# Kernel optimization log

Hardware: AMD Instinct MI355X
Metric: run time of the kernel (lower is better)

## Reference

```python
import jax, jax.numpy as jnp
import numpy as np

# dims: batch, cdd_size, his_size, signal_length, embedding_dim, filter_num, top-k, levels, vocab
B, CDD, HIS, S, E, F, K, L, VOCAB = 32, 5, 50, 20, 300, 150, 30, 3, 50000


def _conv1d(x, w, b, d):
    # x: [N, C_in, S], w: [C_out, C_in, 3], 'same' length via padding=d, dilation=d
    y = jax.lax.conv_general_dilated(x, w, (1,), [(d, d)], rhs_dilation=(d,),
                                     dimension_numbers=('NCW', 'OIW', 'NCW'))
    return y + b[None, :, None]


def _conv3d(x, w, b):
    # x: [N, C_in, D, H, W], padding 1 on all spatial dims
    y = jax.lax.conv_general_dilated(x, w, (1, 1, 1), [(1, 1)] * 3,
                                     dimension_numbers=('NCDHW', 'OIDHW', 'NCDHW'))
    return y + b[None, :, None, None, None]


def _maxpool3(x):
    return jax.lax.reduce_window(x, -jnp.inf, jax.lax.max,
                                 (1, 1, 3, 3, 3), (1, 1, 3, 3, 3), 'VALID')


def setup_inputs() -> dict:
    key = jax.random.key(0)
    ks = jax.random.split(key, 12)
    n = lambda k, s, sc=0.05: jax.random.normal(k, s, dtype=jnp.float32) * sc
    return {
        'candidate_title': jax.random.randint(ks[0], (B, CDD, S), 0, VOCAB),
        'clicked_title': jax.random.randint(ks[1], (B, HIS, S), 0, VOCAB),
        'his_mask': jnp.zeros((B, HIS, 1), dtype=bool),
        'embedding': n(ks[2], (VOCAB, E), 0.1),
        'w1': n(ks[3], (F, E, 3)), 'b1': jnp.zeros((F,), jnp.float32),
        'w2': n(ks[4], (F, F, 3)), 'b2': jnp.zeros((F,), jnp.float32),
        'w3': n(ks[5], (F, F, 3)), 'b3': jnp.zeros((F,), jnp.float32),
        'ln_w': jnp.ones((F,), jnp.float32), 'ln_b': jnp.zeros((F,), jnp.float32),
        'q_words': n(ks[6], (1, F), 1.0), 'q_levels': n(ks[7], (1, F), 1.0),
        'c3d_w1': n(ks[8], (32, L, 3, 3, 3)), 'c3d_b1': jnp.zeros((32,), jnp.float32),
        'c3d_w2': n(ks[9], (16, 32, 3, 3, 3)), 'c3d_b2': jnp.zeros((16,), jnp.float32),
        'ltr_w': n(ks[10], (1, 192)), 'ltr_b': jnp.zeros((1,), jnp.float32),
    }


def reference(candidate_title, clicked_title, his_mask, embedding,
              w1, b1, w2, b2, w3, b3, ln_w, ln_b, q_words, q_levels,
              c3d_w1, c3d_b1, c3d_w2, c3d_b2, ltr_w, ltr_b):
    def ln(x):
        m = x.mean(-1, keepdims=True)
        v = x.var(-1, keepdims=True)  # biased var, matches torch LayerNorm
        return (x - m) / jnp.sqrt(v + 1e-5) * ln_w + ln_b

    scale_e = jnp.sqrt(jnp.float32(E))  # NOTE: original divides by sqrt(embedding_dim)

    def encode(ids):
        nn = ids.shape[1]
        x = embedding[ids].reshape(-1, S, E).transpose(0, 2, 1)  # [N, E, S] (dropout = identity at eval)
        d1 = ln(_conv1d(x, w1, b1, 1).transpose(0, 2, 1))                     # [N, S, F]
        d2 = ln(_conv1d(d1.transpose(0, 2, 1), w2, b2, 2).transpose(0, 2, 1))
        d3 = ln(_conv1d(d2.transpose(0, 2, 1), w3, b3, 3).transpose(0, 2, 1))
        dil = jnp.stack([jax.nn.relu(d1), jax.nn.relu(d2), jax.nn.relu(d3)], axis=2)  # [N, S, L, F]
        dil = dil.reshape(B, nn, S, L, F)
        # level attention with query_levels
        lw = jax.nn.softmax(jnp.einsum('bnslf,f->bnsl', dil, q_levels[0]) / scale_e, axis=-1)
        wf = jnp.einsum('bnsl,bnslf->bnsf', lw, dil)
        # word attention with query_words
        ww = jax.nn.softmax(jnp.einsum('bnsf,f->bns', wf, q_words[0]) / scale_e, axis=-1)
        reprs = jnp.einsum('bns,bnsf->bnf', ww, wf)
        return dil, reprs

    cdd_emb, cdd_repr = encode(candidate_title)   # [B,CDD,S,L,F], [B,CDD,F]
    his_emb, his_repr = encode(clicked_title)     # [B,HIS,S,L,F], [B,HIS,F]

    # news-level attention -> top-k one-hot gating (gather of history news)
    scores = jnp.einsum('bcf,bhf->bch', cdd_repr, his_repr)
    scores = jnp.where(his_mask.transpose(0, 2, 1), -jnp.inf, scores)
    attn = jax.nn.softmax(scores, axis=-1)
    _, idx = jax.lax.top_k(attn, K)                                  # [B,CDD,K]
    his_act = his_emb[jnp.arange(B)[:, None, None], idx]             # [B,CDD,K,S,L,F]

    # fusion tensor: per-level word-word interaction maps
    cdd_t = cdd_emb.transpose(0, 1, 3, 2, 4)       # [B,CDD,L,S,F]
    his_t = his_act.transpose(0, 1, 2, 4, 3, 5)    # [B,CDD,K,L,S,F]
    fusion = jnp.einsum('bclsf,bckltf->bcklst', cdd_t, his_t) / jnp.sqrt(jnp.float32(F))
    fusion = fusion.reshape(B * CDD, K, L, S, S).transpose(0, 2, 1, 3, 4)  # [B*CDD, L, K, S, S]

    h = _maxpool3(jax.nn.relu(_conv3d(fusion, c3d_w1, c3d_b1)))
    h = _maxpool3(jax.nn.relu(_conv3d(h, c3d_w2, c3d_b2)))
    feat = h.reshape(B, CDD, -1)                   # [B, CDD, 192]
    score = jnp.einsum('bcd,d->bc', feat, ltr_w[0]) + ltr_b[0]
    return jax.nn.log_softmax(score, axis=-1)
```

## Files before the change

### kernel.cpp

```cpp
#include <hip/hip_runtime.h>
#include <hip/hip_bf16.h>

#define NB   32
#define NCDD 5
#define NHIS 50
#define SS   20
#define EE   300
#define FF   150
#define KK   30
#define LL   3
#define NSEQ (NB*NCDD + NB*NHIS)
#define NCD  (NB*NCDD)
#define NROW (NSEQ*SS)
#define CONVGRID (NROW/64)

typedef unsigned short u16;
typedef __attribute__((ext_vector_type(8))) short bf16x8;
typedef __attribute__((ext_vector_type(4))) float f32x4;
typedef __attribute__((ext_vector_type(4))) unsigned int u32x4;

__device__ __forceinline__ float b2f(u16 v) {
    union { unsigned int u; float f; } c; c.u = ((unsigned int)v) << 16; return c.f;
}
__device__ __forceinline__ u16 f2b(float f) {
    union { float f; unsigned int u; } c; c.f = f;
    unsigned int r = c.u + 0x7FFF + ((c.u >> 16) & 1);
    return (u16)(r >> 16);
}
__device__ __forceinline__ float ldf(const void* p, size_t i, int isbf) {
    return isbf ? b2f(((const u16*)p)[i]) : ((const float*)p)[i];
}
__device__ __forceinline__ float dget(const float* d, size_t i) {
    unsigned int u = ((const unsigned int*)d)[i];
    return b2f((u16)(u & 0xffffu)) + b2f((u16)(u >> 16));
}
__device__ __forceinline__ bf16x8 ld_frag8(const u16* p) {
    uint2 q0 = *(const uint2*)(p);
    uint2 q1 = *(const uint2*)(p + 4);
    u32x4 t; t.x = q0.x; t.y = q0.y; t.z = q1.x; t.w = q1.y;
    return __builtin_bit_cast(bf16x8, t);
}

__global__ void detect_dtype(const u16* lnw_raw, int* flag) {
    if (threadIdx.x == 0)
        flag[0] = (lnw_raw[0] == 0x3F80 && lnw_raw[1] == 0x3F80) ? 1 : 0;
}

struct CJob { const void* src; float* dst; int n; };
struct CJobs { CJob j[13]; };

__global__ __launch_bounds__(256) void convert_many(CJobs jobs, const int* flagp) {
    int isbf = flagp[0];
    CJob job = jobs.j[blockIdx.x];
    for (int i = threadIdx.x; i < job.n; i += 256) job.dst[i] = ldf(job.src, i, isbf);
}

__global__ __launch_bounds__(256) void repack_wb(const void* w, const int* flagp,
                                                 u16* outh, u16* outl,
                                                 int CIN, int KP, int CV) {
    int isbf = flagp[0];
    int i = blockIdx.x*256 + threadIdx.x;
    if (i >= 160*3*KP) return;
    int g = i % KP; int r = i / KP; int tap = r % 3; int f = r / 3;
    float v = 0.f;
    if (f < FF && g < CV) v = ldf(w, ((size_t)f*CIN + g)*3 + tap, isbf);
    u16 hi = f2b(v);
    u16 lo = f2b(v - b2f(hi));
    size_t o = (size_t)f*(3*KP) + (size_t)tap*KP + g;
    outh[o] = hi; outl[o] = lo;
}

__global__ __launch_bounds__(256) void repack_w1c(const void* w, const int* flagp,
                                                  u16* outh, u16* outl) {
    int isbf = flagp[0];
    int i = blockIdx.x*256 + threadIdx.x;
    if (i >= 3*32*32) return;
    int k = i & 31; int oc = (i >> 5) & 31; int kx = i >> 10;
    float v = 0.f;
    if (k < 27) {
        int kz = k / 9, r = k - kz*9, ky = r / 3, ic = r - ky*3;
        v = ldf(w, ((((size_t)oc*3 + ic)*3 + kz)*3 + ky)*3 + kx, isbf);
    }
    u16 hi = f2b(v); u16 lo = f2b(v - b2f(hi));
    outh[i] = hi; outl[i] = lo;
}

__global__ __launch_bounds__(256) void repack_w2(const void* w, const int* flagp,
                                                 u16* outh, u16* outl) {
    int isbf = flagp[0];
    int i = blockIdx.x*256 + threadIdx.x;
    if (i >= 16*864) return;
    int ic = i & 31; int r = i >> 5; int tap = r % 27; int oc = r / 27;
    float v = ldf(w, ((size_t)oc*32 + ic)*27 + tap, isbf);
    u16 hi = f2b(v); u16 lo = f2b(v - b2f(hi));
    size_t o = (size_t)oc*864 + tap*32 + ic;
    outh[o] = hi; outl[o] = lo;
}

template<int STAGE>
__global__ __launch_bounds__(256) void conv_mfma(const int* __restrict__ flagp,
        const int* __restrict__ cand, const int* __restrict__ clik,
        const void* __restrict__ emb,
        const unsigned int* __restrict__ dprev,
        const u16* __restrict__ wh, const u16* __restrict__ wl,
        const float* __restrict__ bias,
        const float* __restrict__ lnw, const float* __restrict__ lnb,
        unsigned int* __restrict__ dout)
{
    constexpr int KC  = 32;
    constexpr int PAD = 40;
    constexpr int KT  = (STAGE == 0) ? 960 : 480;
    constexpr int NC  = KT / KC;
    constexpr int DIL = (STAGE == 1) ? 2 : 3;
    constexpr int ASZ = 64*PAD, BSZ = 160*PAD;
    constexpr int STG = (2*ASZ + 2*BSZ)*2;
    constexpr int SMB = (STG > 64*164*4) ? STG : 64*164*4;
    __shared__ __align__(16) char smem[SMB];
    u16* Ah = (u16*)smem;
    u16* Al = Ah + ASZ;
    u16* Bh = Al + ASZ;
    u16* Bl = Bh + BSZ;

    const int tid  = threadIdx.x;
    const int row0 = blockIdx.x * 64;
    const int lane = tid & 63, wid = tid >> 6;
    const int wm = wid >> 1, wn = wid & 1;
    const int lr = lane & 15, lk = lane >> 4;
    const int isbf = flagp[0];

    const int arow = tid >> 2, aseg = tid & 3;
    const int grow = row0 + arow;
    const int an   = grow / 20;
    const int as   = grow - an*20;
    int aid[3];
    if constexpr (STAGE == 0) {
        #pragma unroll
        for (int t = 0; t < 3; ++t) {
            int w = as + t - 1;
            aid[t] = ((unsigned)w < 20u) ? ((an < NCD) ? cand[an*SS + w] : clik[(an - NCD)*SS + w])
                                         : -1;
        }
    }

    float xa[8];
    uint4 ra32[2];
    uint4 rb[5];

    auto LOADG = [&](int c) {
        if constexpr (STAGE == 0) {
            int tap = c / 10;
            int e0  = (c - tap*10)*32 + aseg*8;
            int id  = aid[tap];
            float4 x0 = {0.f,0.f,0.f,0.f}, x1 = {0.f,0.f,0.f,0.f};
            if (id >= 0) {
                if (!isbf) {
                    const float* ep = (const float*)emb + (size_t)id*EE + e0;
                    if (e0 < EE)     x0 = *(const float4*)ep;
                    if (e0 + 4 < EE) x1 = *(const float4*)(ep + 4);
                } else {
                    const u16* ep = (const u16*)emb + (size_t)id*EE + e0;
                    float t[8];
                    #pragma unroll
                    for (int j = 0; j < 8; ++j) t[j] = (e0 + j < EE) ? b2f(ep[j]) : 0.f;
                    x0.x=t[0]; x0.y=t[1]; x0.z=t[2]; x0.w=t[3];
                    x1.x=t[4]; x1.y=t[5]; x1.z=t[6]; x1.w=t[7];
                }
            }
            xa[0]=x0.x; xa[1]=x0.y; xa[2]=x0.z; xa[3]=x0.w;
            xa[4]=x1.x; xa[5]=x1.y; xa[6]=x1.z; xa[7]=x1.w;
        } else {
            int tap = c / 5;
            int f0  = (c - tap*5)*32;
            int word = as + DIL*(tap - 1);
            int gbase = f0 + aseg*8;
            ra32[0].x=ra32[0].y=ra32[0].z=ra32[0].w=0u;
            ra32[1].x=ra32[1].y=ra32[1].z=ra32[1].w=0u;
            if ((unsigned)word < 20u && gbase < FF) {
                const unsigned int* p = dprev + (size_t)(an*SS + word)*FF + gbase;
                uint2 q0 = *(const uint2*)(p);
                uint2 q1 = *(const uint2*)(p + 2);
                uint2 q2 = *(const uint2*)(p + 4);
                uint2 q3 = *(const uint2*)(p + 6);
                ra32[0].x = q0.x; ra32[0].y = q0.y; ra32[0].z = q1.x; ra32[0].w = q1.y;
                ra32[1].x = q2.x; ra32[1].y = q2.y; ra32[1].z = q3.x; ra32[1].w = q3.y;
                if (gbase + 7 >= FF) {
                    if (gbase + 1 >= FF) ra32[0].y = 0u;
                    if (gbase + 2 >= FF) ra32[0].z = 0u;
                    if (gbase + 3 >= FF) ra32[0].w = 0u;
                    if (gbase + 4 >= FF) ra32[1].x = 0u;
                    if (gbase + 5 >= FF) ra32[1].y = 0u;
                    if (gbase + 6 >= FF) ra32[1].z = 0u;
                    ra32[1].w = 0u;
                }
            }
        }
        #pragma unroll
        for (int j = 0; j < 5; ++j) {
            int item = tid + j*256;
            const u16* wp = (item < 640) ? wh : wl;
            int rem  = (item < 640) ? item : item - 640;
            rb[j] = *(const uint4*)(wp + (size_t)(rem >> 2)*KT + c*KC + (rem & 3)*8);
        }
    };

    auto WRITE = [&]() {
        uint4 h, l;
        if constexpr (STAGE == 0) {
            u16 hh[8], lo[8];
            #pragma unroll
            for (int j = 0; j < 8; ++j) {
                hh[j] = f2b(xa[j]);
                lo[j] = f2b(xa[j] - b2f(hh[j]));
            }
            h.x = hh[0] | ((unsigned)hh[1] << 16); h.y = hh[2] | ((unsigned)hh[3] << 16);
            h.z = hh[4] | ((unsigned)hh[5] << 16); h.w = hh[6] | ((unsigned)hh[7] << 16);
            l.x = lo[0] | ((unsigned)lo[1] << 16); l.y = lo[2] | ((unsigned)lo[3] << 16);
            l.z = lo[4] | ((unsigned)lo[5] << 16); l.w = lo[6] | ((unsigned)lo[7] << 16);
        } else {
            h.x = (ra32[0].x & 0xffffu) | (ra32[0].y << 16);
            h.y = (ra32[0].z & 0xffffu) | (ra32[0].w << 16);
            h.z = (ra32[1].x & 0xffffu) | (ra32[1].y << 16);
            h.w = (ra32[1].z & 0xffffu) | (ra32[1].w << 16);
            l.x = (ra32[0].x >> 16) | (ra32[0].y & 0xffff0000u);
            l.y = (ra32[0].z >> 16) | (ra32[0].w & 0xffff0000u);
            l.z = (ra32[1].x >> 16) | (ra32[1].y & 0xffff0000u);
            l.w = (ra32[1].z >> 16) | (ra32[1].w & 0xffff0000u);
        }
        *(uint4*)(Ah + arow*PAD + aseg*8) = h;
        *(uint4*)(Al + arow*PAD + aseg*8) = l;
        #pragma unroll
        for (int j = 0; j < 5; ++j) {
            int item = tid + j*256;
            u16* bp = (item < 640) ? Bh : Bl;
            int rem = (item < 640) ? item : item - 640;
            *(uint4*)(bp + (rem >> 2)*PAD + (rem & 3)*8) = rb[j];
        }
    };

    f32x4 acc[2][5];
    #pragma unroll
    for (int mf = 0; mf < 2; ++mf)
        #pragma unroll
        for (int nf = 0; nf < 5; ++nf)
            acc[mf][nf] = (f32x4){0.f,0.f,0.f,0.f};

    auto COMPUTE = [&]() {
        bf16x8 fah[2], fal[2], fbh[5], fbl[5];
        #pragma unroll
        for (int mf = 0; mf < 2; ++mf) {
            fah[mf] = *(const bf16x8*)(Ah + (wm*32 + mf*16 + lr)*PAD + lk*8);
            fal[mf] = *(const bf16x8*)(Al + (wm*32 + mf*16 + lr)*PAD + lk*8);
        }
        #pragma unroll
        for (int nf = 0; nf < 5; ++nf) {
            fbh[nf] = *(const bf16x8*)(Bh + (wn*80 + nf*16 + lr)*PAD + lk*8);
            fbl[nf] = *(const bf16x8*)(Bl + (wn*80 + nf*16 + lr)*PAD + lk*8);
        }
        #pragma unroll
        for (int mf = 0; mf < 2; ++mf)
            #pragma unroll
            for (int nf = 0; nf < 5; ++nf)
                acc[mf][nf] = __builtin_amdgcn_mfma_f32_16x16x32_bf16(fah[mf], fbh[nf], acc[mf][nf], 0, 0, 0);
        #pragma unroll
        for (int mf = 0; mf < 2; ++mf)
            #pragma unroll
            for (int nf = 0; nf < 5; ++nf)
                acc[mf][nf] = __builtin_amdgcn_mfma_f32_16x16x32_bf16(fah[mf], fbl[nf], acc[mf][nf], 0, 0, 0);
        #pragma unroll
        for (int mf = 0; mf < 2; ++mf)
            #pragma unroll
            for (int nf = 0; nf < 5; ++nf)
                acc[mf][nf] = __builtin_amdgcn_mfma_f32_16x16x32_bf16(fal[mf], fbh[nf], acc[mf][nf], 0, 0, 0);
    };

    LOADG(0); WRITE();
    for (int c = 0; c < NC; ++c) {
        if (c + 1 < NC) LOADG(c + 1);
        __syncthreads();
        COMPUTE();
        __syncthreads();
        if (c + 1 < NC) WRITE();
    }

    float* outb = (float*)smem;
    #pragma unroll
    for (int mf = 0; mf < 2; ++mf)
        #pragma unroll
        for (int nf = 0; nf < 5; ++nf)
            #pragma unroll
            for (int r = 0; r < 4; ++r)
                outb[(wm*32 + mf*16 + lk*4 + r)*164 + wn*80 + nf*16 + lr] = acc[mf][nf][r];
    __syncthreads();

    for (int rl = wid*16; rl < wid*16 + 16; ++rl) {
        float vv[3]; float sum = 0.f, sq = 0.f;
        #pragma unroll
        for (int j = 0; j < 3; ++j) {
            int f = lane + j*64;
            float v = 0.f;
            if (f < FF) v = outb[rl*164 + f] + bias[f];
            vv[j] = v; sum += v; sq += v*v;
        }
        #pragma unroll
        for (int off = 32; off; off >>= 1) { sum += __shfl_down(sum, off); sq += __shfl_down(sq, off); }
        sum = __shfl(sum, 0); sq = __shfl(sq, 0);
        float m = sum / FF, var = sq / FF - m*m, inv = rsqrtf(var + 1e-5f);
        #pragma unroll
        for (int j = 0; j < 3; ++j) {
            int f = lane + j*64;
            if (f < FF) {
                float v = (vv[j] - m) * inv * lnw[f] + lnb[f];
                u16 hi = f2b(v);
                unsigned int lo = (unsigned int)f2b(v - b2f(hi));
                dout[(size_t)(row0 + rl)*FF + f] = (unsigned int)hi | (lo << 16);
            }
        }
    }
}

__global__ __launch_bounds__(256) void lvwd_attn(const float* d1, const float* d2, const float* d3,
                                                 const float* ql, const float* qw, float* reprs) {
    __shared__ float wfs[SS*FF];
    __shared__ float scs[SS];
    int n = blockIdx.x, tid = threadIdx.x;
    int wave = tid >> 6, lane = tid & 63;
    for (int s = wave; s < SS; s += 4) {
        size_t base = ((size_t)n*SS + s) * FF;
        float v[3][3];
        float dt[3] = {0.f, 0.f, 0.f};
        #pragma unroll
        for (int j = 0; j < 3; ++j) {
            int f = lane + j*64;
            float q = (f < FF) ? ql[f] : 0.f;
            float x0 = (f < FF) ? fmaxf(dget(d1, base+f), 0.f) : 0.f;
            float x1 = (f < FF) ? fmaxf(dget(d2, base+f), 0.f) : 0.f;
            float x2 = (f < FF) ? fmaxf(dget(d3, base+f), 0.f) : 0.f;
            v[0][j] = x0; v[1][j] = x1; v[2][j] = x2;
            dt[0] += x0*q; dt[1] += x1*q; dt[2] += x2*q;
        }
        #pragma unroll
        for (int off = 32; off; off >>= 1) {
            dt[0] += __shfl_xor(dt[0], off);
            dt[1] += __shfl_xor(dt[1], off);
            dt[2] += __shfl_xor(dt[2], off);
        }
        const float sc = 0.057735026918962584f;
        float a0 = dt[0]*sc, a1 = dt[1]*sc, a2 = dt[2]*sc;
        float mx = fmaxf(a0, fmaxf(a1, a2));
        float e0 = expf(a0-mx), e1 = expf(a1-mx), e2 = expf(a2-mx);
        float den = e0+e1+e2;
        float l0 = e0/den, l1 = e1/den, l2 = e2/den;
        #pragma unroll
        for (int j = 0; j < 3; ++j) {
            int f = lane + j*64;
            if (f < FF) wfs[s*FF + f] = l0*v[0][j] + l1*v[1][j] + l2*v[2][j];
        }
    }
    __syncthreads();
    if (wave == 0) {
        if (lane < SS) {
            float a = 0.f;
            for (int f = 0; f < FF; ++f) a += wfs[lane*FF + f]*qw[f];
            scs[lane] = a * 0.057735026918962584f;
        }
        float mx = -1e30f;
        #pragma unroll
        for (int s = 0; s < SS; ++s) mx = fmaxf(mx, scs[s]);
        float ww[SS]; float den = 0.f;
        #pragma unroll
        for (int s = 0; s < SS; ++s) { ww[s] = expf(scs[s]-mx); den += ww[s]; }
        float inv = 1.f/den;
        for (int f = lane; f < FF; f += 64) {
            float a = 0.f;
            #pragma unroll
            for (int s = 0; s < SS; ++s) a += ww[s]*wfs[s*FF + f];
            reprs[(size_t)n*FF + f] = a*inv;
        }
    }
}

__global__ __launch_bounds__(256) void score_kernel(const float* reprs, const unsigned char* mask,
                                                    float* scores) {
    int i = blockIdx.x*256 + threadIdx.x;
    if (i >= NB*NCDD*NHIS) return;
    int b = i/(NCDD*NHIS); int r = i%(NCDD*NHIS); int h = r%NHIS; int c = r/NHIS;
    const float* cr = reprs + (size_t)(b*NCDD + c)*FF;
    const float* hr = reprs + (size_t)(NCD + b*NHIS + h)*FF;
    float a = 0.f;
    for (int f = 0; f < FF; ++f) a += cr[f]*hr[f];
    if (mask[b*NHIS + h]) a = -1e30f;
    scores[i] = a;
}

__global__ __launch_bounds__(64) void topk_kernel(const float* scores, int* idx) {
    int i = blockIdx.x*64 + threadIdx.x;
    if (i >= NB*NCDD) return;
    float sc[NHIS];
    const float* sp = scores + i*NHIS;
    for (int h = 0; h < NHIS; ++h) sc[h] = sp[h];
    for (int k = 0; k < KK; ++k) {
        int best = 0; float bv = -1e38f;
        for (int h = 0; h < NHIS; ++h) { if (sc[h] > bv) { bv = sc[h]; best = h; } }
        idx[i*KK + k] = best;
        sc[best] = -1e38f;
    }
}

__global__ __launch_bounds__(256) void fusion_kernel(const float* d1, const float* d2, const float* d3,
                                                     const int* idx, unsigned int* fusp) {
    constexpr int RS  = 168;
    constexpr int TSZ = 32*RS;
    __shared__ __align__(16) u16 smem[4*TSZ];
    u16* Ah = smem;
    u16* Al = smem + TSZ;
    u16* Hh = smem + 2*TSZ;
    u16* Hl = smem + 3*TSZ;
    int blk = blockIdx.x;
    int k = blk % KK; int r2 = blk / KK; int l = r2 % LL; int bc = r2 / LL;
    int b = bc / NCDD;
    int nh = NCD + b*NHIS + idx[bc*KK + k];
    const float* dl = (l == 0) ? d1 : ((l == 1) ? d2 : d3);
    const unsigned int* Ap = (const unsigned int*)dl + (size_t)bc*SS*FF;
    const unsigned int* Hp = (const unsigned int*)dl + (size_t)nh*SS*FF;
    int tid = threadIdx.x;
    for (int i = tid; i < 4*TSZ/8; i += 256)
        *(uint4*)(smem + (size_t)i*8) = (uint4){0u,0u,0u,0u};
    __syncthreads();
    for (int item = tid; item < 760; item += 256) {
        int side = item >= 380;
        int rem  = side ? item - 380 : item;
        int row  = rem / 19, f0 = (rem - row*19)*8;
        const unsigned int* p = (side ? Hp : Ap) + row*FF + f0;
        unsigned int q[8];
        #pragma unroll
        for (int j = 0; j < 8; j += 2) {
            uint2 t2 = {0u, 0u};
            if (f0 + j < FF) t2 = *(const uint2*)(p + j);
            q[j] = t2.x; q[j+1] = t2.y;
        }
        unsigned int hh[8], ll[8];
        #pragma unroll
        for (int j = 0; j < 8; ++j) {
            unsigned int u = q[j];
            float f = b2f((u16)(u & 0xffffu)) + b2f((u16)(u >> 16));
            int keep = (f > 0.f);
            hh[j] = keep ? (u & 0xffffu) : 0u;
            ll[j] = keep ? (u >> 16)     : 0u;
        }
        uint4 h, lo;
        h.x  = hh[0] | (hh[1] << 16); h.y  = hh[2] | (hh[3] << 16);
        h.z  = hh[4] | (hh[5] << 16); h.w  = hh[6] | (hh[7] << 16);
        lo.x = ll[0] | (ll[1] << 16); lo.y = ll[2] | (ll[3] << 16);
        lo.z = ll[4] | (ll[5] << 16); lo.w = ll[6] | (ll[7] << 16);
        u16* dh = (side ? Hh : Ah) + row*RS + f0;
        u16* dL = (side ? Hl : Al) + row*RS + f0;
        *(uint4*)dh = h;
        *(uint4*)dL = lo;
    }
    __syncthreads();
    const int lane = tid & 63, wid = tid >> 6;
    const int wm = wid >> 1, wn = wid & 1;
    const int lr = lane & 15, lk = lane >> 4;
    f32x4 acc = {0.f, 0.f, 0.f, 0.f};
    #pragma unroll
    for (int c = 0; c < 5; ++c) {
        bf16x8 fah = *(const bf16x8*)(Ah + (wm*16 + lr)*RS + c*32 + lk*8);
        bf16x8 fal = *(const bf16x8*)(Al + (wm*16 + lr)*RS + c*32 + lk*8);
        bf16x8 fbh = *(const bf16x8*)(Hh + (wn*16 + lr)*RS + c*32 + lk*8);
        bf16x8 fbl = *(const bf16x8*)(Hl + (wn*16 + lr)*RS + c*32 + lk*8);
        acc = __builtin_amdgcn_mfma_f32_16x16x32_bf16(fah, fbh, acc, 0, 0, 0);
        acc = __builtin_amdgcn_mfma_f32_16x16x32_bf16(fah, fbl, acc, 0, 0, 0);
        acc = __builtin_amdgcn_mfma_f32_16x16x32_bf16(fal, fbh, acc, 0, 0, 0);
    }
    #pragma unroll
    for (int r = 0; r < 4; ++r) {
        int s = wm*16 + lk*4 + r, t = wn*16 + lr;
        if (s < SS && t < SS) {
            float v = acc[r] * 0.08164965809277261f;
            u16 hi = f2b(v);
            unsigned int lo = (unsigned int)f2b(v - b2f(hi));
            fusp[(size_t)blk*400 + s*20 + t] = (unsigned int)hi | (lo << 16);
        }
    }
}

#define C1RS 36
__global__ __launch_bounds__(256) void c3d1_mfma(const unsigned int* __restrict__ fusp,
                                                 const u16* __restrict__ wh,
                                                 const u16* __restrict__ wl,
                                                 const float* __restrict__ bias,
                                                 unsigned int* __restrict__ h1p) {
    __shared__ __align__(16) u16 Ah[209*C1RS];
    __shared__ __align__(16) u16 Al[209*C1RS];
    __shared__ int mb[18*32];
    int blk = blockIdx.x;
    int yh = blk & 1; int r0 = blk >> 1; int g = r0 % 10; int bc = r0 / 10;
    int tid = threadIdx.x;
    for (int i = tid; i < 18*32; i += 256) mb[i] = 0;
    for (int i = tid; i < 209*C1RS; i += 256) { Ah[i] = 0; Al[i] = 0; }
    const int lane = tid & 63, wid = tid >> 6;
    const int lr = lane & 15, lk = lane >> 4;
    const float b0 = bias[lr], b1 = bias[16 + lr];
    const int p  = tid;
    const int yp = p / 22, cx = p - yp*22;
    const int gx = cx - 1;
    const int yb = yh*9 + yp - 1;
    const bool prow = (p < 198);
    const bool gxok = ((unsigned)gx < 20u);

    for (int zi = 0; zi < 3; ++zi) {
        int z = g*3 + zi;
        __syncthreads();
        if (p < 208) {
            #pragma unroll
            for (int k = 0; k < 27; ++k) {
                const int kz = k / 9, r2 = k - kz*9, ky = r2 / 3, ic = r2 - ky*3;
                int zz = z + kz - 1;
                int gy = yb + ky;
                unsigned int u = 0;
                if (prow && gxok && (unsigned)gy < 20u && (unsigned)zz < 30u)
                    u = fusp[((size_t)(bc*3 + ic)*30 + zz)*400 + gy*20 + gx];
                Ah[p*C1RS + k] = (u16)(u & 0xffffu);
                Al[p*C1RS + k] = (u16)(u >> 16);
            }
        }
        __syncthreads();
        f32x4 acc[4][2];
        #pragma unroll
        for (int fi = 0; fi < 4; ++fi) { acc[fi][0] = (f32x4){0,0,0,0}; acc[fi][1] = (f32x4){0,0,0,0}; }
        #pragma unroll
        for (int kx = 0; kx < 3; ++kx) {
            bf16x8 bh0 = *(const bf16x8*)(wh + kx*1024 + lr*32 + lk*8);
            bf16x8 bl0 = *(const bf16x8*)(wl + kx*1024 + lr*32 + lk*8);
            bf16x8 bh1 = *(const bf16x8*)(wh + kx*1024 + (16 + lr)*32 + lk*8);
            bf16x8 bl1 = *(const bf16x8*)(wl + kx*1024 + (16 + lr)*32 + lk*8);
            #pragma unroll
            for (int fi = 0; fi < 4; ++fi) {
                int frag = wid + fi*4;
                if (frag >= 13) break;
                int pp = frag*16 + lr + (kx - 1);
                int adr = (pp < 0 ? 0 : pp)*C1RS + lk*8;
                bf16x8 ah = ld_frag8(Ah + adr);
                bf16x8 al = ld_frag8(Al + adr);
                acc[fi][0] = __builtin_amdgcn_mfma_f32_16x16x32_bf16(ah, bh0, acc[fi][0], 0, 0, 0);
                acc[fi][0] = __builtin_amdgcn_mfma_f32_16x16x32_bf16(ah, bl0, acc[fi][0], 0, 0, 0);
                acc[fi][0] = __builtin_amdgcn_mfma_f32_16x16x32_bf16(al, bh0, acc[fi][0], 0, 0, 0);
                acc[fi][1] = __builtin_amdgcn_mfma_f32_16x16x32_bf16(ah, bh1, acc[fi][1], 0, 0, 0);
                acc[fi][1] = __builtin_amdgcn_mfma_f32_16x16x32_bf16(ah, bl1, acc[fi][1], 0, 0, 0);
                acc[fi][1] = __builtin_amdgcn_mfma_f32_16x16x32_bf16(al, bh1, acc[fi][1], 0, 0, 0);
            }
        }
        #pragma unroll
        for (int fi = 0; fi < 4; ++fi) {
            int frag = wid + fi*4;
            if (frag >= 13) break;
            #pragma unroll
            for (int r4 = 0; r4 < 4; ++r4) {
                int pc = frag*16 + lk*4 + r4;
                if (pc >= 198) continue;
                int ypc = pc / 22, cxc = pc - ypc*22;
                int gxc = cxc - 1;
                if ((unsigned)gxc < 18u) {
                    int cell = (ypc/3)*6 + gxc/3;
                    float v0 = fmaxf(acc[fi][0][r4] + b0, 0.f);
                    float v1 = fmaxf(acc[fi][1][r4] + b1, 0.f);
                    atomicMax(&mb[cell*32 + lr],      __float_as_int(v0));
                    atomicMax(&mb[cell*32 + 16 + lr], __float_as_int(v1));
                }
            }
        }
    }
    __syncthreads();
    for (int i = tid; i < 18*32; i += 256) {
        int oc = i & 31, cell = i >> 5;
        int dyl = cell / 6, dx = cell - dyl*6;
        int dydx = (yh*3 + dyl)*6 + dx;
        float v = __int_as_float(mb[i]);
        u16 hi = f2b(v);
        unsigned int lo = (unsigned int)f2b(v - b2f(hi));
        h1p[((size_t)(bc*10 + g)*36 + dydx)*32 + oc] = (unsigned int)hi | (lo << 16);
    }
}

#define ARS 36
#define APL (36*ARS)
__global__ __launch_bounds__(256) void c3d2_kernel(const unsigned int* __restrict__ h1p,
                                                   const u16* __restrict__ wh,
                                                   const u16* __restrict__ wl,
                                                   const float* __restrict__ bias,
                                                   float* __restrict__ h2) {
    __shared__ __align__(16) u16 Ah[12*APL];
    __shared__ __align__(16) u16 Al[12*APL];
    int bc = blockIdx.x, tid = threadIdx.x;
    for (int i = tid; i < 2*APL; i += 256) {
        int a = (i < APL) ? i : (11*APL + i - APL);
        Ah[a] = 0; Al[a] = 0;
    }
    for (int i = tid; i < 10*36*32; i += 256) {
        int ic = i & 31; int r = i >> 5; int yx = r % 36; int z = r / 36;
        unsigned int u = h1p[(size_t)bc*11520 + i];
        int a = (z + 1)*APL + yx*ARS + ic;
        Ah[a] = (u16)(u & 0xffffu);
        Al[a] = (u16)(u >> 16);
    }
    __syncthreads();
    const int lane = tid & 63, wid = tid >> 6;
    const int lr = lane & 15, lk = lane >> 4;
    const int t0 = wid*6;
    int rr[6], rz[6], ry[6], rx[6];
    #pragma unroll
    for (int ti = 0; ti < 6; ++ti) {
        int r = (t0 + ti)*16 + lr;
        rr[ti] = r;
        int z = r / 36; int yx = r - z*36; int y = yx / 6;
        rz[ti] = z; ry[ti] = y; rx[ti] = yx - y*6;
    }
    f32x4 acc[6];
    #pragma unroll
    for (int ti = 0; ti < 6; ++ti) acc[ti] = (f32x4){0.f,0.f,0.f,0.f};
    for (int tap = 0; tap < 27; ++tap) {
        int kz = tap/9, kyx = tap - kz*9, ky = kyx/3, kx = kyx - ky*3;
        bf16x8 fbh = *(const bf16x8*)(wh + (size_t)lr*864 + tap*32 + lk*8);
        bf16x8 fbl = *(const bf16x8*)(wl + (size_t)lr*864 + tap*32 + lk*8);
        #pragma unroll
        for (int ti = 0; ti < 6; ++ti) {
            int yy = ry[ti] + ky - 1;
            int xx = rx[ti] + kx - 1;
            bool ok = (rr[ti] < 360) && ((unsigned)yy < 6u) && ((unsigned)xx < 6u);
            int a = ok ? ((rz[ti] + kz)*APL + (yy*6 + xx)*ARS + lk*8) : (lk*8);
            bf16x8 fah = ld_frag8(Ah + a);
            bf16x8 fal = ld_frag8(Al + a);
            acc[ti] = __builtin_amdgcn_mfma_f32_16x16x32_bf16(fah, fbh, acc[ti], 0, 0, 0);
            acc[ti] = __builtin_amdgcn_mfma_f32_16x16x32_bf16(fah, fbl, acc[ti], 0, 0, 0);
            acc[ti] = __builtin_amdgcn_mfma_f32_16x16x32_bf16(fal, fbh, acc[ti], 0, 0, 0);
        }
    }
    float b = bias[lr];
    #pragma unroll
    for (int ti = 0; ti < 6; ++ti) {
        #pragma unroll
        for (int r4 = 0; r4 < 4; ++r4) {
            int row = (t0 + ti)*16 + lk*4 + r4;
            if (row < 360)
                h2[((size_t)bc*16 + lr)*360 + row] = fmaxf(acc[ti][r4] + b, 0.f);
        }
    }
}

__global__ __launch_bounds__(256) void pool2_kernel(const float* h2, float* h2p) {
    int i = blockIdx.x*256 + threadIdx.x;
    if (i >= NCD*16*3*2*2) return;
    int dx = i % 2; int r = i/2;
    int dy = r % 2; r /= 2;
    int dz = r % 3; r /= 3;
    int oc = r % 16; r /= 16;
    int bc = r;
    const float* hp = h2 + ((size_t)bc*16 + oc)*360;
    float best = -1e30f;
    for (int pz = 0; pz < 3; ++pz)
    for (int py = 0; py < 3; ++py)
    for (int px = 0; px < 3; ++px) {
        int z = dz*3+pz, y = dy*3+py, x = dx*3+px;
        best = fmaxf(best, hp[(z*6 + y)*6 + x]);
    }
    h2p[i] = best;
}

__global__ __launch_bounds__(64) void ltr_kernel(const float* h2p, const float* lw,
                                                 const float* lb, float* sc) {
    int i = blockIdx.x*64 + threadIdx.x;
    if (i >= NB*NCDD) return;
    const float* f = h2p + (size_t)i*192;
    float a = lb[0];
    for (int d = 0; d < 192; ++d) a += f[d]*lw[d];
    sc[i] = a;
}

__global__ __launch_bounds__(64) void lsm_kernel(const float* sc, const int* flagp, void* out) {
    int b = threadIdx.x;
    if (b >= NB) return;
    int isbf = flagp[0];
    float v[NCDD]; float mx = -1e30f;
    #pragma unroll
    for (int c = 0; c < NCDD; ++c) { v[c] = sc[b*NCDD + c]; mx = fmaxf(mx, v[c]); }
    float den = 0.f;
    #pragma unroll
    for (int c = 0; c < NCDD; ++c) den += expf(v[c]-mx);
    float lse = mx + logf(den);
    #pragma unroll
    for (int c = 0; c < NCDD; ++c) {
        float o = v[c] - lse;
        if (isbf) ((u16*)out)[b*NCDD + c] = f2b(o);
        else      ((float*)out)[b*NCDD + c] = o;
    }
}

extern "C" void kernel_launch(void* const* d_in, const int* in_sizes, int n_in,
                              void* d_out, int out_size, void* d_ws, size_t ws_size,
                              hipStream_t stream) {
    const int* cand  = (const int*)d_in[0];
    const int* clik  = (const int*)d_in[1];
    const unsigned char* mask = (const unsigned char*)d_in[2];
    const void* emb  = d_in[3];
    const void* w1   = d_in[4];
    const void* b1   = d_in[5];
    const void* w2   = d_in[6];
    const void* b2   = d_in[7];
    const void* w3   = d_in[8];
    const void* b3   = d_in[9];
    const void* lnw  = d_in[10];
    const void* lnb  = d_in[11];
    const void* qw   = d_in[12];
    const void* ql   = d_in[13];
    const void* cw1  = d_in[14];
    const void* cb1  = d_in[15];
    const void* cw2  = d_in[16];
    const void* cb2  = d_in[17];
    const void* lw   = d_in[18];
    const void* lb   = d_in[19];

    char* wsb = (char*)d_ws;
    size_t off = 0;
    auto A = [&](size_t bytes) -> void* {
        void* p = wsb + off;
        off = (off + bytes + 255) & ~(size_t)255;
        return p;
    };
    int*   flag = (int*)A(4);
    float* b1f  = (float*)A(FF*4);
    float* b2f  = (float*)A(FF*4);
    float* b3f  = (float*)A(FF*4);
    float* lnwf = (float*)A(FF*4);
    float* lnbf = (float*)A(FF*4);
    float* qwf  = (float*)A(FF*4);
    float* qlf  = (float*)A(FF*4);
    float* c1w  = (float*)A(32*3*27*4);
    float* c1b  = (float*)A(32*4);
    float* c2w  = (float*)A(16*32*27*4);
    float* c2b  = (float*)A(16*4);
    float* lwf  = (float*)A(192*4);
    float* lbf  = (float*)A(4);
    u16*   wt1h = (u16*)A((size_t)160*960*2);
    u16*   wt1l = (u16*)A((size_t)160*960*2);
    u16*   wt2h = (u16*)A((size_t)160*480*2);
    u16*   wt2l = (u16*)A((size_t)160*480*2);
    u16*   wt3h = (u16*)A((size_t)160*480*2);
    u16*   wt3l = (u16*)A((size_t)160*480*2);
    u16*   w1ch = (u16*)A((size_t)3*32*32*2);
    u16*   w1cl = (u16*)A((size_t)3*32*32*2);
    u16*   w2ch = (u16*)A((size_t)16*864*2);
    u16*   w2cl = (u16*)A((size_t)16*864*2);
    float* d1   = (float*)A((size_t)NSEQ*SS*FF*4);
    float* d2   = (float*)A((size_t)NSEQ*SS*FF*4);
    float* d3   = (float*)A((size_t)NSEQ*SS*FF*4);
    unsigned int* fusp = (unsigned int*)A((size_t)NCD*LL*KK*SS*SS*4);
    float* reprs= (float*)A((size_t)NSEQ*FF*4);
    float* scb  = (float*)A((size_t)NB*NCDD*NHIS*4);
    int*   idx  = (int*)A((size_t)NB*NCDD*KK*4);
    unsigned int* h1p = (unsigned int*)d1;
    float* h2   = d2;
    float* h2p  = d3;
    float* fsc  = (float*)((char*)d3 + 256*1024);
    (void)ws_size; (void)in_sizes; (void)n_in; (void)out_size;

    detect_dtype<<<1, 64, 0, stream>>>((const u16*)lnw, flag);

    CJobs jobs;
    jobs.j[0]  = {b1,  b1f,  FF};
    jobs.j[1]  = {b2,  b2f,  FF};
    jobs.j[2]  = {b3,  b3f,  FF};
    jobs.j[3]  = {lnw, lnwf, FF};
    jobs.j[4]  = {lnb, lnbf, FF};
    jobs.j[5]  = {qw,  qwf,  FF};
    jobs.j[6]  = {ql,  qlf,  FF};
    jobs.j[7]  = {cw1, c1w,  32*3*27};
    jobs.j[8]  = {cb1, c1b,  32};
    jobs.j[9]  = {cw2, c2w,  16*32*27};
    jobs.j[10] = {cb2, c2b,  16};
    jobs.j[11] = {lw,  lwf,  192};
    jobs.j[12] = {lb,  lbf,  1};
    convert_many<<<13, 256, 0, stream>>>(jobs, flag);
    repack_wb<<<(160*960 + 255)/256, 256, 0, stream>>>(w1, flag, wt1h, wt1l, EE, 320, 300);
    repack_wb<<<(160*480 + 255)/256, 256, 0, stream>>>(w2, flag, wt2h, wt2l, FF, 160, 150);
    repack_wb<<<(160*480 + 255)/256, 256, 0, stream>>>(w3, flag, wt3h, wt3l, FF, 160, 150);
    repack_w1c<<<(3*32*32 + 255)/256, 256, 0, stream>>>(cw1, flag, w1ch, w1cl);
    repack_w2<<<(16*864 + 255)/256, 256, 0, stream>>>(cw2, flag, w2ch, w2cl);

    conv_mfma<0><<<CONVGRID, 256, 0, stream>>>(flag, cand, clik, emb, nullptr,
                                               wt1h, wt1l, b1f, lnwf, lnbf, (unsigned int*)d1);
    conv_mfma<1><<<CONVGRID, 256, 0, stream>>>(flag, cand, clik, emb, (const unsigned int*)d1,
                                               wt2h, wt2l, b2f, lnwf, lnbf, (unsigned int*)d2);
    conv_mfma<2><<<CONVGRID, 256, 0, stream>>>(flag, cand, clik, emb, (const unsigned int*)d2,
                                               wt3h, wt3l, b3f, lnwf, lnbf, (unsigned int*)d3);

    lvwd_attn<<<NSEQ, 256, 0, stream>>>(d1, d2, d3, qlf, qwf, reprs);
    score_kernel<<<(NB*NCDD*NHIS + 255)/256, 256, 0, stream>>>(reprs, mask, scb);
    topk_kernel<<<(NB*NCDD + 63)/64, 64, 0, stream>>>(scb, idx);
    fusion_kernel<<<NCD*LL*KK, 256, 0, stream>>>(d1, d2, d3, idx, fusp);
    c3d1_mfma<<<NCD*10*2, 256, 0, stream>>>(fusp, w1ch, w1cl, c1b, h1p);
    c3d2_kernel<<<NCD, 256, 0, stream>>>(h1p, w2ch, w2cl, c2b, h2);
    pool2_kernel<<<(NCD*16*3*2*2 + 255)/256, 256, 0, stream>>>(h2, h2p);
    ltr_kernel<<<(NB*NCDD + 63)/64, 64, 0, stream>>>(h2p, lwf, lbf, fsc);
    lsm_kernel<<<1, 64, 0, stream>>>(fsc, flag, d_out);
}
```

Measured before the change: 775.1 us.

## Read conv weight fragments directly from global and double-buffer A tiles

Weight (B operand) tiles are no longer staged through shared memory. Each wave now loads its bf16 hi/lo weight fragments straight from global memory (expected to hit cache) inside the compute step. The A tile is double-buffered in LDS, so each chunk needs one barrier instead of two. This cuts LDS traffic and synchronisation, at the cost of more global/L2 loads that are now exposed on the MFMA critical path.

Result: faster. 704.2 us (-9.1%).

```diff
diff --git a/kernel.cpp b/kernel.cpp
--- a/kernel.cpp
+++ b/kernel.cpp
@@ -107,19 +107,15 @@
         const float* __restrict__ lnw, const float* __restrict__ lnb,
         unsigned int* __restrict__ dout)
 {
-    constexpr int KC  = 32;
-    constexpr int PAD = 40;
-    constexpr int KT  = (STAGE == 0) ? 960 : 480;
-    constexpr int NC  = KT / KC;
-    constexpr int DIL = (STAGE == 1) ? 2 : 3;
-    constexpr int ASZ = 64*PAD, BSZ = 160*PAD;
-    constexpr int STG = (2*ASZ + 2*BSZ)*2;
-    constexpr int SMB = (STG > 64*164*4) ? STG : 64*164*4;
+    constexpr int KC   = 32;
+    constexpr int PAD  = 40;
+    constexpr int KT   = (STAGE == 0) ? 960 : 480;
+    constexpr int NC   = KT / KC;
+    constexpr int DIL  = (STAGE == 1) ? 2 : 3;
+    constexpr int ABUF = 64*PAD;
+    constexpr int SMB  = 64*164*4;
     __shared__ __align__(16) char smem[SMB];
-    u16* Ah = (u16*)smem;
-    u16* Al = Ah + ASZ;
-    u16* Bh = Al + ASZ;
-    u16* Bl = Bh + BSZ;
+    u16* Ab = (u16*)smem;
 
     const int tid  = threadIdx.x;
     const int row0 = blockIdx.x * 64;
@@ -132,25 +128,22 @@
     const int grow = row0 + arow;
     const int an   = grow / 20;
     const int as   = grow - an*20;
-    int aid[3];
+    int aid0 = -1, aid1 = -1, aid2 = -1;
     if constexpr (STAGE == 0) {
-        #pragma unroll
-        for (int t = 0; t < 3; ++t) {
-            int w = as + t - 1;
-            aid[t] = ((unsigned)w < 20u) ? ((an < NCD) ? cand[an*SS + w] : clik[(an - NCD)*SS + w])
-                                         : -1;
-        }
+        int w0 = as - 1, w2 = as + 1;
+        aid0 = ((unsigned)w0 < 20u) ? ((an < NCD) ? cand[an*SS + w0] : clik[(an - NCD)*SS + w0]) : -1;
+        aid1 = (an < NCD) ? cand[an*SS + as] : clik[(an - NCD)*SS + as];
+        aid2 = ((unsigned)w2 < 20u) ? ((an < NCD) ? cand[an*SS + w2] : clik[(an - NCD)*SS + w2]) : -1;
     }
 
     float xa[8];
     uint4 ra32[2];
-    uint4 rb[5];
 
     auto LOADG = [&](int c) {
         if constexpr (STAGE == 0) {
             int tap = c / 10;
             int e0  = (c - tap*10)*32 + aseg*8;
-            int id  = aid[tap];
+            int id  = (tap == 0) ? aid0 : ((tap == 1) ? aid1 : aid2);
             float4 x0 = {0.f,0.f,0.f,0.f}, x1 = {0.f,0.f,0.f,0.f};
             if (id >= 0) {
                 if (!isbf) {
@@ -194,16 +187,11 @@
                 }
             }
         }
-        #pragma unroll
-        for (int j = 0; j < 5; ++j) {
-            int item = tid + j*256;
-            const u16* wp = (item < 640) ? wh : wl;
-            int rem  = (item < 640) ? item : item - 640;
-            rb[j] = *(const uint4*)(wp + (size_t)(rem >> 2)*KT + c*KC + (rem & 3)*8);
-        }
     };
 
-    auto WRITE = [&]() {
+    auto WRITEA = [&](int b) {
+        u16* Ah = Ab + b*(2*ABUF);
+        u16* Al = Ah + ABUF;
         uint4 h, l;
         if constexpr (STAGE == 0) {
             u16 hh[8], lo[8];
@@ -228,13 +216,6 @@
         }
         *(uint4*)(Ah + arow*PAD + aseg*8) = h;
         *(uint4*)(Al + arow*PAD + aseg*8) = l;
-        #pragma unroll
-        for (int j = 0; j < 5; ++j) {
-            int item = tid + j*256;
-            u16* bp = (item < 640) ? Bh : Bl;
-            int rem = (item < 640) ? item : item - 640;
-            *(uint4*)(bp + (rem >> 2)*PAD + (rem & 3)*8) = rb[j];
-        }
     };
 
     f32x4 acc[2][5];
@@ -244,7 +225,9 @@
         for (int nf = 0; nf < 5; ++nf)
             acc[mf][nf] = (f32x4){0.f,0.f,0.f,0.f};
 
-    auto COMPUTE = [&]() {
+    auto COMPUTE = [&](int b, int c) {
+        const u16* Ah = Ab + b*(2*ABUF);
+        const u16* Al = Ah + ABUF;
         bf16x8 fah[2], fal[2], fbh[5], fbl[5];
         #pragma unroll
         for (int mf = 0; mf < 2; ++mf) {
@@ -253,8 +236,9 @@
         }
         #pragma unroll
         for (int nf = 0; nf < 5; ++nf) {
-            fbh[nf] = *(const bf16x8*)(Bh + (wn*80 + nf*16 + lr)*PAD + lk*8);
-            fbl[nf] = *(const bf16x8*)(Bl + (wn*80 + nf*16 + lr)*PAD + lk*8);
+            size_t bo = (size_t)(wn*80 + nf*16 + lr)*KT + c*KC + lk*8;
+            fbh[nf] = *(const bf16x8*)(wh + bo);
+            fbl[nf] = *(const bf16x8*)(wl + bo);
         }
         #pragma unroll
         for (int mf = 0; mf < 2; ++mf)
@@ -273,13 +257,13 @@
                 acc[mf][nf] = __builtin_amdgcn_mfma_f32_16x16x32_bf16(fal[mf], fbh[nf], acc[mf][nf], 0, 0, 0);
     };
 
-    LOADG(0); WRITE();
+    LOADG(0); WRITEA(0);
+    __syncthreads();
     for (int c = 0; c < NC; ++c) {
         if (c + 1 < NC) LOADG(c + 1);
+        COMPUTE(c & 1, c);
+        if (c + 1 < NC) WRITEA((c + 1) & 1);
         __syncthreads();
-        COMPUTE();
-        __syncthreads();
-        if (c + 1 < NC) WRITE();
     }
 
     float* outb = (float*)smem;
```
